# Kernel optimization log

Measured on AMD Instinct MI355X. Metric: run time of the kernel, lower is better.

The kernel has to match this reference:

```python
import jax, jax.numpy as jnp
import numpy as np

B, A, D, H, F = 256, 96, 384, 192, 96   # molecules, atoms, feat, hidden, species-MLP out
S = 4                                   # number of species (H, C, N, O)
E = B * A * 32                          # edges (avg degree 32)
CUTOFF = 5.2


def smooth_cutoff(d, cutoff):
    # Smoothstep-style cutoff: 1 at d=0, smoothly -> 0 at d=cutoff (Smoothstep class, reversed edges)
    x = jnp.clip((cutoff - d) / cutoff, 0.0, 1.0)
    return x ** 3 * (x * (6.0 * x - 15.0) + 10.0)


def setup_inputs() -> dict:
    key = jax.random.key(0)
    ks = jax.random.split(key, 9)
    species = jax.random.randint(ks[0], (B, A), 0, S, dtype=jnp.int32)
    in_features = jax.random.normal(ks[1], (B, A, D), dtype=jnp.float32)
    atom_index12 = jax.random.randint(ks[2], (2, E), 0, B * A, dtype=jnp.int32)
    distances = jax.random.uniform(ks[3], (E,), jnp.float32, 0.1, CUTOFF)
    total_charges = jnp.zeros((B,), jnp.float32)
    W1 = jax.random.normal(ks[4], (S, D, H), jnp.float32) / np.float32(np.sqrt(D))
    W2 = jax.random.normal(ks[5], (S, H, F), jnp.float32) / np.float32(np.sqrt(H))
    Wn = jax.random.normal(ks[6], (S, F, F), jnp.float32) / np.float32(np.sqrt(F))
    Wf = jax.random.normal(ks[7], (S, 2 * F, 1), jnp.float32) / np.float32(np.sqrt(2 * F))
    return dict(species=species, in_features=in_features, atom_index12=atom_index12,
                distances=distances, total_charges=total_charges,
                W1=W1, W2=W2, Wn=Wn, Wf=Wf,
                decay_prefactor=jnp.asarray(1.0, jnp.float32),
                decay_factor=jnp.asarray(1.0, jnp.float32))


def reference(species, in_features, atom_index12, distances, total_charges,
              W1, W2, Wn, Wf, decay_prefactor, decay_factor):
    b, a, d = in_features.shape
    n = b * a
    sp = species.reshape(-1)                      # [N]
    x = in_features.reshape(n, d)                 # [N, D]

    # per-species main MLP dispatch: internal[i] = MLP_{sp[i]}(x[i])
    internal = jnp.zeros((n, F), x.dtype)
    for s in range(S):
        mask = (sp == s)[:, None]
        h = jax.nn.gelu(x @ W1[s]) @ W2[s]        # [N, F]
        internal = internal + jnp.where(mask, h, jnp.zeros((), x.dtype))

    # per-species neighbor MLP
    nbr = jnp.zeros((n, F), x.dtype)
    for s in range(S):
        mask = (sp == s)[:, None]
        nbr = nbr + jnp.where(mask, internal @ Wn[s], jnp.zeros((), x.dtype))

    # distance-decayed edge messages: merged[i0] += nbr[i1]*w, merged[i1] += nbr[i0]*w
    decay = (decay_prefactor ** 2) * jnp.exp(-(decay_factor ** 2) * distances) \
            * smooth_cutoff(distances, CUTOFF)    # [E]
    i0, i1 = atom_index12[0], atom_index12[1]
    m_to_i0 = nbr[i1] * decay[:, None]            # [E, F]
    m_to_i1 = nbr[i0] * decay[:, None]
    merged = jax.ops.segment_sum(jnp.concatenate([m_to_i0, m_to_i1], axis=0),
                                 jnp.concatenate([i0, i1], axis=0),
                                 num_segments=n)  # [N, F]

    feats = jnp.concatenate([internal, merged], axis=-1)  # [N, 2F]

    # per-species final head -> precharges
    precharges = jnp.zeros((n,), x.dtype)
    for s in range(S):
        mask = (sp == s)
        precharges = precharges + jnp.where(mask, (feats @ Wf[s])[:, 0], jnp.zeros((), x.dtype))
    precharges = precharges.reshape(b, a)

    # total-charge redistribution (uniform factors, no learned redistribution)
    dummy_mask = species != -1
    factors = 1.0 / dummy_mask.sum(-1, keepdims=True).astype(x.dtype)
    charges = precharges + (total_charges - precharges.sum(-1))[:, None] * factors
    charges = jnp.where(dummy_mask, charges, jnp.zeros((), x.dtype))
    return species, charges, precharges
```

## Files before the change

kernel.cpp:

```cpp
#include <hip/hip_runtime.h>
#include <cstdint>
#include <cstddef>

#define NBm 256
#define NAm 96
#define NDm 384
#define NHm 192
#define NFm 96
#define NSm 4
#define NATOMS (NBm*NAm)
#define NEe (NATOMS*32)
#define NMSG (2*NEe)
#define HBLK2 768
#define CUTOFF_ 5.2f

typedef __attribute__((ext_vector_type(8))) short short8;
typedef __attribute__((ext_vector_type(4))) float float4v;
typedef __attribute__((ext_vector_type(2))) int int2v;

__device__ __forceinline__ short f2bf(float f){
  union { float f; unsigned u; } v; v.f = f;
  unsigned r = v.u + 0x7FFFu + ((v.u >> 16) & 1u);
  return (short)(r >> 16);
}

__device__ __forceinline__ float gelu_t(float x){
  float u = 0.7978845608028654f * (x + 0.044715f * x*x*x);
  float e = __expf(-2.0f * fabsf(u));
  float t = (1.0f - e) / (1.0f + e);
  t = (u >= 0.f) ? t : -t;
  return 0.5f * x * (1.0f + t);
}

#define W1N (NSm*NDm*NHm)
#define W2N (NSm*NHm*NFm)
#define WNN (NSm*NFm*NFm)
__global__ void k_wprep(const float* __restrict__ W1, const float* __restrict__ W2,
                        const float* __restrict__ Wn,
                        short* __restrict__ W1t, short* __restrict__ W2t,
                        short* __restrict__ Wnt, int* __restrict__ spc){
  if (blockIdx.x == 0 && threadIdx.x < NSm) spc[threadIdx.x] = 0;
  int idx = blockIdx.x*256 + threadIdx.x;
  if (idx < W1N){
    int s = idx / (NDm*NHm); int rem = idx - s*NDm*NHm;
    int k = rem / NHm, c = rem - k*NHm;
    W1t[(s*NHm + c)*NDm + k] = f2bf(W1[idx]);
  } else if (idx < W1N + W2N){
    int j = idx - W1N;
    int s = j / (NHm*NFm); int rem = j - s*NHm*NFm;
    int k = rem / NFm, c = rem - k*NFm;
    W2t[(s*NFm + c)*NHm + k] = f2bf(W2[j]);
  } else if (idx < W1N + W2N + WNN){
    int j = idx - W1N - W2N;
    int s = j / (NFm*NFm); int rem = j - s*NFm*NFm;
    int k = rem / NFm, c = rem - k*NFm;
    Wnt[(s*NFm + c)*NFm + k] = f2bf(Wn[j]);
  }
}

__global__ void k_spcount(const int* __restrict__ sp, int* __restrict__ spc){
  __shared__ int h[NSm];
  int t = threadIdx.x;
  if (t < NSm) h[t] = 0;
  __syncthreads();
  int i = blockIdx.x*256 + t;
  atomicAdd(&h[sp[i]], 1);
  __syncthreads();
  if (t < NSm) atomicAdd(&spc[t], h[t]);
}

__global__ void k_spscan(const int* __restrict__ spc, int* __restrict__ sps, int* __restrict__ spcur){
  if (threadIdx.x==0 && blockIdx.x==0){
    int r=0;
    for (int s=0;s<NSm;s++){ sps[s]=r; spcur[s]=r; r+=spc[s]; }
    sps[NSm]=r;
  }
}

__global__ void k_spscatter(const int* __restrict__ sp, int* __restrict__ spcur,
                            int* __restrict__ order){
  __shared__ int h[NSm], base[NSm];
  int t = threadIdx.x;
  if (t < NSm) h[t]=0;
  __syncthreads();
  int i = blockIdx.x*256 + t;
  int s = sp[i];
  int lr = atomicAdd(&h[s], 1);
  __syncthreads();
  if (t < NSm) base[t] = atomicAdd(&spcur[t], h[t]);
  __syncthreads();
  order[base[s] + lr] = i;
}

__global__ __launch_bounds__(256) void k_mlp(
    const float* __restrict__ X, const int* __restrict__ order,
    const int* __restrict__ sps,
    const short* __restrict__ W1t, const short* __restrict__ W2t,
    const short* __restrict__ Wnt, const float* __restrict__ Wf,
    float* __restrict__ pre, float* __restrict__ nbr_g){
  const int s = blockIdx.y;
  const int s0 = sps[s];
  const int cnt = sps[s+1] - s0;
  const int row0 = blockIdx.x * 64;
  if (row0 >= cnt) return;

  __shared__ short Hs[64][200];
  __shared__ short Is[64][104];
  __shared__ short Ws[19968];
  __shared__ int aids[64];

  const int tid = threadIdx.x;
  if (tid < 64){
    int r = row0 + tid;
    aids[tid] = order[s0 + ((r < cnt) ? r : 0)];
  }
  __syncthreads();

  const int wave = tid >> 6, lane = tid & 63;
  const int lrow = lane & 15, quad = lane >> 4;
  const int arow = wave*16 + lrow;
  const float* xrow = X + (size_t)aids[arow]*NDm + quad*8;

  short8 afs[12];
  #pragma unroll
  for (int kb=0; kb<12; kb++){
    const float* p = xrow + kb*32;
    #pragma unroll
    for (int j=0;j<8;j++) afs[kb][j] = f2bf(p[j]);
  }

  const short* W1s = W1t + (size_t)s*NHm*NDm;
  float4v acc[12];
  #pragma unroll
  for (int i=0;i<12;i++){ acc[i][0]=0.f; acc[i][1]=0.f; acc[i][2]=0.f; acc[i][3]=0.f; }
  for (int kc=0; kc<4; kc++){
    __syncthreads();
    for (int e = tid; e < 192*12; e += 256){
      int c = e / 12, u = e - c*12;
      *(short8*)(&Ws[c*104 + u*8]) = *(const short8*)(W1s + c*NDm + kc*96 + u*8);
    }
    __syncthreads();
    #pragma unroll
    for (int kb3=0; kb3<3; kb3++){
      short8 af = afs[kc*3 + kb3];
      #pragma unroll
      for (int ct=0; ct<12; ct++){
        short8 bfb = *(const short8*)(&Ws[(ct*16 + lrow)*104 + kb3*32 + quad*8]);
        acc[ct] = __builtin_amdgcn_mfma_f32_16x16x32_bf16(af, bfb, acc[ct], 0,0,0);
      }
    }
  }
  #pragma unroll
  for (int ct=0; ct<12; ct++){
    #pragma unroll
    for (int r=0;r<4;r++){
      Hs[wave*16 + quad*4 + r][ct*16 + lrow] = f2bf(gelu_t(acc[ct][r]));
    }
  }

  const short* W2s = W2t + (size_t)s*NFm*NHm;
  float4v acc2[6];
  #pragma unroll
  for (int i=0;i<6;i++){ acc2[i][0]=0.f; acc2[i][1]=0.f; acc2[i][2]=0.f; acc2[i][3]=0.f; }
  __syncthreads();
  for (int e = tid; e < 96*24; e += 256){
    int c = e / 24, u = e - c*24;
    *(short8*)(&Ws[c*200 + u*8]) = *(const short8*)(W2s + c*NHm + u*8);
  }
  __syncthreads();
  for (int kb=0; kb<6; kb++){
    short8 af2 = *(const short8*)(&Hs[wave*16 + lrow][kb*32 + quad*8]);
    #pragma unroll
    for (int ct=0; ct<6; ct++){
      short8 bfb = *(const short8*)(&Ws[(ct*16 + lrow)*200 + kb*32 + quad*8]);
      acc2[ct] = __builtin_amdgcn_mfma_f32_16x16x32_bf16(af2, bfb, acc2[ct], 0,0,0);
    }
  }
  #pragma unroll
  for (int ct=0; ct<6; ct++){
    #pragma unroll
    for (int r=0;r<4;r++){
      Is[wave*16 + quad*4 + r][ct*16 + lrow] = f2bf(acc2[ct][r]);
    }
  }

  {
    float pr[4] = {0.f,0.f,0.f,0.f};
    #pragma unroll
    for (int ct=0; ct<6; ct++){
      float wv = Wf[s*2*NFm + ct*16 + lrow];
      #pragma unroll
      for (int r=0;r<4;r++) pr[r] += acc2[ct][r] * wv;
    }
    #pragma unroll
    for (int m=1; m<16; m<<=1){
      #pragma unroll
      for (int r=0;r<4;r++) pr[r] += __shfl_xor(pr[r], m, 64);
    }
    if (lrow == 0){
      #pragma unroll
      for (int r=0;r<4;r++){
        int row = wave*16 + quad*4 + r;
        if (row0 + row < cnt) pre[aids[row]] = pr[r];
      }
    }
  }

  const short* Wns = Wnt + (size_t)s*NFm*NFm;
  float4v acc3[6];
  #pragma unroll
  for (int i=0;i<6;i++){ acc3[i][0]=0.f; acc3[i][1]=0.f; acc3[i][2]=0.f; acc3[i][3]=0.f; }
  __syncthreads();
  for (int e = tid; e < 96*12; e += 256){
    int c = e / 12, u = e - c*12;
    *(short8*)(&Ws[c*104 + u*8]) = *(const short8*)(Wns + c*NFm + u*8);
  }
  __syncthreads();
  for (int kb=0; kb<3; kb++){
    short8 af3 = *(const short8*)(&Is[wave*16 + lrow][kb*32 + quad*8]);
    #pragma unroll
    for (int ct=0; ct<6; ct++){
      short8 bfb = *(const short8*)(&Ws[(ct*16 + lrow)*104 + kb*32 + quad*8]);
      acc3[ct] = __builtin_amdgcn_mfma_f32_16x16x32_bf16(af3, bfb, acc3[ct], 0,0,0);
    }
  }
  #pragma unroll
  for (int ct=0; ct<6; ct++){
    #pragma unroll
    for (int r=0;r<4;r++){
      int row = wave*16 + quad*4 + r, col = ct*16 + lrow;
      if (row0 + row < cnt) nbr_g[(size_t)aids[row]*NFm + col] = acc3[ct][r];
    }
  }
}

__global__ void k_nd4(const float* __restrict__ nbr, const float* __restrict__ Wf,
                      float* __restrict__ nd4){
  int a = blockIdx.x*4 + (threadIdx.x >> 6);
  int lane = threadIdx.x & 63;
  bool lo = lane < 32;
  const float* np = nbr + (size_t)a*NFm;
  float nv1 = np[lane];
  float nv2 = lo ? np[64+lane] : 0.f;
  const float* w0 = Wf + 0*2*NFm + NFm;
  const float* w1 = Wf + 1*2*NFm + NFm;
  const float* w2 = Wf + 2*2*NFm + NFm;
  const float* w3 = Wf + 3*2*NFm + NFm;
  float n0 = nv1*w0[lane] + (lo ? nv2*w0[64+lane] : 0.f);
  float n1 = nv1*w1[lane] + (lo ? nv2*w1[64+lane] : 0.f);
  float n2 = nv1*w2[lane] + (lo ? nv2*w2[64+lane] : 0.f);
  float n3 = nv1*w3[lane] + (lo ? nv2*w3[64+lane] : 0.f);
  #pragma unroll
  for (int m=1; m<64; m<<=1){
    n0 += __shfl_xor(n0, m, 64);
    n1 += __shfl_xor(n1, m, 64);
    n2 += __shfl_xor(n2, m, 64);
    n3 += __shfl_xor(n3, m, 64);
  }
  if (lane == 0){
    float4v v; v[0]=n0; v[1]=n1; v[2]=n2; v[3]=n3;
    *(float4v*)(nd4 + (size_t)a*4) = v;
  }
}

__global__ __launch_bounds__(1024) void k_hist(const int* __restrict__ ai,
                                               int* __restrict__ Hist){
  __shared__ int h[NBm];
  int t = threadIdx.x;
  if (t < NBm) h[t] = 0;
  __syncthreads();
  int base = blockIdx.x*2048;
  atomicAdd(&h[ai[base + t] / NAm], 1);
  atomicAdd(&h[ai[base + 1024 + t] / NAm], 1);
  __syncthreads();
  if (t < NBm) Hist[blockIdx.x*NBm + t] = h[t];
}

__global__ void k_mscan(int* __restrict__ Hist, int* __restrict__ Tot){
  __shared__ int sums[256];
  int mol = blockIdx.x, t = threadIdx.x;
  int v[3]; int loc = 0;
  #pragma unroll
  for (int j=0;j<3;j++){ v[j] = Hist[(t*3+j)*NBm + mol]; loc += v[j]; }
  sums[t] = loc; __syncthreads();
  for (int off=1; off<256; off<<=1){
    int x = (t >= off) ? sums[t-off] : 0;
    __syncthreads();
    sums[t] += x;
    __syncthreads();
  }
  int run = sums[t] - loc;
  #pragma unroll
  for (int j=0;j<3;j++){ Hist[(t*3+j)*NBm + mol] = run; run += v[j]; }
  if (t == 255) Tot[mol] = run;
}

__global__ void k_segscan(const int* __restrict__ Tot, int* __restrict__ Seg){
  __shared__ int s[256];
  int t = threadIdx.x;
  int v = Tot[t]; s[t] = v; __syncthreads();
  for (int off=1; off<256; off<<=1){
    int x = (t >= off) ? s[t-off] : 0;
    __syncthreads();
    s[t] += x;
    __syncthreads();
  }
  Seg[t] = s[t] - v;
  if (t == 255) Seg[256] = s[255];
}

__global__ __launch_bounds__(1024) void k_scatter(const int* __restrict__ ai,
    const float* __restrict__ dist, const float* __restrict__ pref,
    const float* __restrict__ fac, const int* __restrict__ Hist,
    const int* __restrict__ Seg, int2v* __restrict__ Msg){
  __shared__ int cnt[NBm];
  __shared__ int off[NBm];
  int t = threadIdx.x;
  if (t < NBm){ cnt[t] = 0; off[t] = Seg[t] + Hist[blockIdx.x*NBm + t]; }
  __syncthreads();
  int base = blockIdx.x*2048;
  float p = pref[0], fc = fac[0];
  #pragma unroll
  for (int half=0; half<2; half++){
    int m = base + half*1024 + t;
    int dest = ai[m];
    int other = ai[(m < NEe) ? m + NEe : m - NEe];
    int e = (m < NEe) ? m : m - NEe;
    float d = dist[e];
    float x = (CUTOFF_ - d) * (1.0f/CUTOFF_);
    x = fminf(fmaxf(x, 0.f), 1.f);
    float sc = x*x*x*(x*(6.f*x - 15.f) + 10.f);
    float w = p*p * expf(-fc*fc*d) * sc;
    int mol = dest / NAm, dl = dest - mol*NAm;
    int rank = atomicAdd(&cnt[mol], 1);
    int2v msg; msg[0] = (other << 7) | dl; msg[1] = __float_as_int(w);
    Msg[off[mol] + rank] = msg;
  }
}

__global__ __launch_bounds__(1024) void k_accum(const int* __restrict__ Seg,
    const int2v* __restrict__ Msg, const float* __restrict__ nd4,
    const int* __restrict__ sp, const float* __restrict__ pre,
    const float* __restrict__ tc, float* __restrict__ out){
  __shared__ float acc[NAm];
  __shared__ int spl[NAm];
  __shared__ float red[128];
  int mol = blockIdx.x, t = threadIdx.x;
  if (t < NAm){ acc[t] = 0.f; spl[t] = sp[mol*NAm + t]; }
  __syncthreads();
  int s0 = Seg[mol], s1 = Seg[mol+1];
  for (int i = s0 + t; i < s1; i += 1024){
    int2v kw = Msg[i];
    int key = kw[0]; float w = __int_as_float(kw[1]);
    int dl = key & 127, other = key >> 7;
    float val = w * nd4[(size_t)other*4 + spl[dl]];
    atomicAdd(&acc[dl], val);
  }
  __syncthreads();
  float pch = 0.f;
  if (t < NAm) pch = pre[mol*NAm + t] + acc[t];
  if (t < 128) red[t] = (t < NAm) ? pch : 0.f;
  __syncthreads();
  for (int o=64; o>0; o>>=1){
    if (t < o) red[t] += red[t + o];
    __syncthreads();
  }
  float sum = red[0];
  if (t < NAm){
    float c = pch + (tc[mol] - sum) * (1.0f/96.0f);
    out[mol*NAm + t] = (float)spl[t];
    out[NATOMS + mol*NAm + t] = c;
    out[2*NATOMS + mol*NAm + t] = pch;
  }
}

extern "C" void kernel_launch(void* const* d_in, const int* in_sizes, int n_in,
                              void* d_out, int out_size, void* d_ws, size_t ws_size,
                              hipStream_t stream) {
  const int*   species = (const int*)  d_in[0];
  const float* X       = (const float*)d_in[1];
  const int*   ai      = (const int*)  d_in[2];
  const float* dist    = (const float*)d_in[3];
  const float* tc      = (const float*)d_in[4];
  const float* W1      = (const float*)d_in[5];
  const float* W2      = (const float*)d_in[6];
  const float* Wn      = (const float*)d_in[7];
  const float* Wf      = (const float*)d_in[8];
  const float* pref    = (const float*)d_in[9];
  const float* fac     = (const float*)d_in[10];
  float* out = (float*)d_out;

  char* w = (char*)d_ws;
  auto alloc = [&](size_t bytes)->char*{
    char* p = w; w += (bytes + 255) & ~(size_t)255; return p;
  };
  int*   spc   = (int*)  alloc(64);
  int*   sps   = (int*)  alloc(64);
  int*   spcur = (int*)  alloc(64);
  int*   order = (int*)  alloc((size_t)NATOMS*4);
  float* nd4   = (float*)alloc((size_t)NATOMS*4*4);
  float* pre   = (float*)alloc((size_t)NATOMS*4);
  float* nbr   = (float*)alloc((size_t)NATOMS*NFm*4);
  short* W1t   = (short*)alloc((size_t)W1N*2);
  short* W2t   = (short*)alloc((size_t)W2N*2);
  short* Wnt   = (short*)alloc((size_t)WNN*2);
  int*   Hist  = (int*)  alloc((size_t)HBLK2*NBm*4);
  int*   Tot   = (int*)  alloc(1024);
  int*   Seg   = (int*)  alloc((NBm+1)*4);
  int2v* Msg   = (int2v*)alloc((size_t)NMSG*8);

  k_wprep<<<(W1N+W2N+WNN)/256, 256, 0, stream>>>(W1, W2, Wn, W1t, W2t, Wnt, spc);
  k_spcount<<<NATOMS/256, 256, 0, stream>>>(species, spc);
  k_spscan<<<1, 64, 0, stream>>>(spc, sps, spcur);
  k_spscatter<<<NATOMS/256, 256, 0, stream>>>(species, spcur, order);
  dim3 g(NATOMS/64, NSm);
  k_mlp<<<g, 256, 0, stream>>>(X, order, sps, W1t, W2t, Wnt, Wf, pre, nbr);
  k_nd4<<<NATOMS/4, 256, 0, stream>>>(nbr, Wf, nd4);
  k_hist<<<HBLK2, 1024, 0, stream>>>(ai, Hist);
  k_mscan<<<NBm, 256, 0, stream>>>(Hist, Tot);
  k_segscan<<<1, 256, 0, stream>>>(Tot, Seg);
  k_scatter<<<HBLK2, 1024, 0, stream>>>(ai, dist, pref, fac, Hist, Seg, Msg);
  k_accum<<<NBm, 1024, 0, stream>>>(Seg, Msg, nd4, species, pre, tc, out);
}
```

Measured before the change: 182.6 us.

## Replace sort-by-molecule edge pipeline with direct global atomic accumulation

Drops the histogram, scan and scatter kernels that bucketed messages by molecule. Each edge now computes its decay weight once and atomically adds both directed contributions straight into a global per-atom buffer, which is zeroed inside the weight-prep kernel. This removes several launches and the 12.6 MB message buffer write and read. In exchange it relies on global float atomics on random addresses, which can contend and makes the summation order nondeterministic.

New measurement: 253.1 us. 1.39x slower.

```diff
diff --git a/kernel.cpp b/kernel.cpp
--- a/kernel.cpp
+++ b/kernel.cpp
@@ -10,13 +10,10 @@
 #define NSm 4
 #define NATOMS (NBm*NAm)
 #define NEe (NATOMS*32)
-#define NMSG (2*NEe)
-#define HBLK2 768
 #define CUTOFF_ 5.2f
 
 typedef __attribute__((ext_vector_type(8))) short short8;
 typedef __attribute__((ext_vector_type(4))) float float4v;
-typedef __attribute__((ext_vector_type(2))) int int2v;
 
 __device__ __forceinline__ short f2bf(float f){
   union { float f; unsigned u; } v; v.f = f;
@@ -35,10 +32,12 @@
 #define W1N (NSm*NDm*NHm)
 #define W2N (NSm*NHm*NFm)
 #define WNN (NSm*NFm*NFm)
+#define WTOT (W1N+W2N+WNN)
 __global__ void k_wprep(const float* __restrict__ W1, const float* __restrict__ W2,
                         const float* __restrict__ Wn,
                         short* __restrict__ W1t, short* __restrict__ W2t,
-                        short* __restrict__ Wnt, int* __restrict__ spc){
+                        short* __restrict__ Wnt, int* __restrict__ spc,
+                        float* __restrict__ mrg){
   if (blockIdx.x == 0 && threadIdx.x < NSm) spc[threadIdx.x] = 0;
   int idx = blockIdx.x*256 + threadIdx.x;
   if (idx < W1N){
@@ -50,11 +49,14 @@
     int s = j / (NHm*NFm); int rem = j - s*NHm*NFm;
     int k = rem / NFm, c = rem - k*NFm;
     W2t[(s*NFm + c)*NHm + k] = f2bf(W2[j]);
-  } else if (idx < W1N + W2N + WNN){
+  } else if (idx < WTOT){
     int j = idx - W1N - W2N;
     int s = j / (NFm*NFm); int rem = j - s*NFm*NFm;
     int k = rem / NFm, c = rem - k*NFm;
     Wnt[(s*NFm + c)*NFm + k] = f2bf(Wn[j]);
+  } else {
+    int z = idx - WTOT;
+    mrg[z] = 0.f;
   }
 }
 
@@ -263,103 +265,37 @@
   }
 }
 
-__global__ __launch_bounds__(1024) void k_hist(const int* __restrict__ ai,
-                                               int* __restrict__ Hist){
-  __shared__ int h[NBm];
-  int t = threadIdx.x;
-  if (t < NBm) h[t] = 0;
-  __syncthreads();
-  int base = blockIdx.x*2048;
-  atomicAdd(&h[ai[base + t] / NAm], 1);
-  atomicAdd(&h[ai[base + 1024 + t] / NAm], 1);
-  __syncthreads();
-  if (t < NBm) Hist[blockIdx.x*NBm + t] = h[t];
-}
-
-__global__ void k_mscan(int* __restrict__ Hist, int* __restrict__ Tot){
-  __shared__ int sums[256];
-  int mol = blockIdx.x, t = threadIdx.x;
-  int v[3]; int loc = 0;
-  #pragma unroll
-  for (int j=0;j<3;j++){ v[j] = Hist[(t*3+j)*NBm + mol]; loc += v[j]; }
-  sums[t] = loc; __syncthreads();
-  for (int off=1; off<256; off<<=1){
-    int x = (t >= off) ? sums[t-off] : 0;
-    __syncthreads();
-    sums[t] += x;
-    __syncthreads();
-  }
-  int run = sums[t] - loc;
-  #pragma unroll
-  for (int j=0;j<3;j++){ Hist[(t*3+j)*NBm + mol] = run; run += v[j]; }
-  if (t == 255) Tot[mol] = run;
-}
-
-__global__ void k_segscan(const int* __restrict__ Tot, int* __restrict__ Seg){
-  __shared__ int s[256];
-  int t = threadIdx.x;
-  int v = Tot[t]; s[t] = v; __syncthreads();
-  for (int off=1; off<256; off<<=1){
-    int x = (t >= off) ? s[t-off] : 0;
-    __syncthreads();
-    s[t] += x;
-    __syncthreads();
-  }
-  Seg[t] = s[t] - v;
-  if (t == 255) Seg[256] = s[255];
-}
-
-__global__ __launch_bounds__(1024) void k_scatter(const int* __restrict__ ai,
+__global__ __launch_bounds__(256) void k_edges(const int* __restrict__ ai,
     const float* __restrict__ dist, const float* __restrict__ pref,
-    const float* __restrict__ fac, const int* __restrict__ Hist,
-    const int* __restrict__ Seg, int2v* __restrict__ Msg){
-  __shared__ int cnt[NBm];
-  __shared__ int off[NBm];
-  int t = threadIdx.x;
-  if (t < NBm){ cnt[t] = 0; off[t] = Seg[t] + Hist[blockIdx.x*NBm + t]; }
-  __syncthreads();
-  int base = blockIdx.x*2048;
+    const float* __restrict__ fac, const int* __restrict__ sp,
+    const float* __restrict__ nd4, float* __restrict__ mrg){
+  int e = blockIdx.x*256 + threadIdx.x;
+  int i0 = ai[e];
+  int i1 = ai[NEe + e];
+  float d = dist[e];
   float p = pref[0], fc = fac[0];
-  #pragma unroll
-  for (int half=0; half<2; half++){
-    int m = base + half*1024 + t;
-    int dest = ai[m];
-    int other = ai[(m < NEe) ? m + NEe : m - NEe];
-    int e = (m < NEe) ? m : m - NEe;
-    float d = dist[e];
-    float x = (CUTOFF_ - d) * (1.0f/CUTOFF_);
-    x = fminf(fmaxf(x, 0.f), 1.f);
-    float sc = x*x*x*(x*(6.f*x - 15.f) + 10.f);
-    float w = p*p * expf(-fc*fc*d) * sc;
-    int mol = dest / NAm, dl = dest - mol*NAm;
-    int rank = atomicAdd(&cnt[mol], 1);
-    int2v msg; msg[0] = (other << 7) | dl; msg[1] = __float_as_int(w);
-    Msg[off[mol] + rank] = msg;
-  }
-}
-
-__global__ __launch_bounds__(1024) void k_accum(const int* __restrict__ Seg,
-    const int2v* __restrict__ Msg, const float* __restrict__ nd4,
-    const int* __restrict__ sp, const float* __restrict__ pre,
+  float x = (CUTOFF_ - d) * (1.0f/CUTOFF_);
+  x = fminf(fmaxf(x, 0.f), 1.f);
+  float sc = x*x*x*(x*(6.f*x - 15.f) + 10.f);
+  float w = p*p * expf(-fc*fc*d) * sc;
+  int s0 = sp[i0], s1 = sp[i1];
+  float v0 = w * nd4[(size_t)i1*4 + s0];
+  float v1 = w * nd4[(size_t)i0*4 + s1];
+  atomicAdd(&mrg[i0], v0);
+  atomicAdd(&mrg[i1], v1);
+}
+
+__global__ __launch_bounds__(128) void k_final(const float* __restrict__ pre,
+    const float* __restrict__ mrg, const int* __restrict__ sp,
     const float* __restrict__ tc, float* __restrict__ out){
-  __shared__ float acc[NAm];
-  __shared__ int spl[NAm];
   __shared__ float red[128];
   int mol = blockIdx.x, t = threadIdx.x;
-  if (t < NAm){ acc[t] = 0.f; spl[t] = sp[mol*NAm + t]; }
-  __syncthreads();
-  int s0 = Seg[mol], s1 = Seg[mol+1];
-  for (int i = s0 + t; i < s1; i += 1024){
-    int2v kw = Msg[i];
-    int key = kw[0]; float w = __int_as_float(kw[1]);
-    int dl = key & 127, other = key >> 7;
-    float val = w * nd4[(size_t)other*4 + spl[dl]];
-    atomicAdd(&acc[dl], val);
-  }
-  __syncthreads();
-  float pch = 0.f;
-  if (t < NAm) pch = pre[mol*NAm + t] + acc[t];
-  if (t < 128) red[t] = (t < NAm) ? pch : 0.f;
+  float pch = 0.f; int s = 0;
+  if (t < NAm){
+    s = sp[mol*NAm + t];
+    pch = pre[mol*NAm + t] + mrg[mol*NAm + t];
+  }
+  red[t] = (t < NAm) ? pch : 0.f;
   __syncthreads();
   for (int o=64; o>0; o>>=1){
     if (t < o) red[t] += red[t + o];
@@ -367,9 +303,8 @@
   }
   float sum = red[0];
   if (t < NAm){
-    float c = pch + (tc[mol] - sum) * (1.0f/96.0f);
-    out[mol*NAm + t] = (float)spl[t];
-    out[NATOMS + mol*NAm + t] = c;
+    out[mol*NAm + t] = (float)s;
+    out[NATOMS + mol*NAm + t] = pch + (tc[mol] - sum) * (1.0f/96.0f);
     out[2*NATOMS + mol*NAm + t] = pch;
   }
 }
@@ -400,25 +335,19 @@
   int*   order = (int*)  alloc((size_t)NATOMS*4);
   float* nd4   = (float*)alloc((size_t)NATOMS*4*4);
   float* pre   = (float*)alloc((size_t)NATOMS*4);
+  float* mrg   = (float*)alloc((size_t)NATOMS*4);
   float* nbr   = (float*)alloc((size_t)NATOMS*NFm*4);
   short* W1t   = (short*)alloc((size_t)W1N*2);
   short* W2t   = (short*)alloc((size_t)W2N*2);
   short* Wnt   = (short*)alloc((size_t)WNN*2);
-  int*   Hist  = (int*)  alloc((size_t)HBLK2*NBm*4);
-  int*   Tot   = (int*)  alloc(1024);
-  int*   Seg   = (int*)  alloc((NBm+1)*4);
-  int2v* Msg   = (int2v*)alloc((size_t)NMSG*8);
-
-  k_wprep<<<(W1N+W2N+WNN)/256, 256, 0, stream>>>(W1, W2, Wn, W1t, W2t, Wnt, spc);
+
+  k_wprep<<<WTOT/256 + NATOMS/256, 256, 0, stream>>>(W1, W2, Wn, W1t, W2t, Wnt, spc, mrg);
   k_spcount<<<NATOMS/256, 256, 0, stream>>>(species, spc);
   k_spscan<<<1, 64, 0, stream>>>(spc, sps, spcur);
   k_spscatter<<<NATOMS/256, 256, 0, stream>>>(species, spcur, order);
   dim3 g(NATOMS/64, NSm);
   k_mlp<<<g, 256, 0, stream>>>(X, order, sps, W1t, W2t, Wnt, Wf, pre, nbr);
   k_nd4<<<NATOMS/4, 256, 0, stream>>>(nbr, Wf, nd4);
-  k_hist<<<HBLK2, 1024, 0, stream>>>(ai, Hist);
-  k_mscan<<<NBm, 256, 0, stream>>>(Hist, Tot);
-  k_segscan<<<1, 256, 0, stream>>>(Tot, Seg);
-  k_scatter<<<HBLK2, 1024, 0, stream>>>(ai, dist, pref, fac, Hist, Seg, Msg);
-  k_accum<<<NBm, 1024, 0, stream>>>(Seg, Msg, nd4, species, pre, tc, out);
-}
+  k_edges<<<NEe/256, 256, 0, stream>>>(ai, dist, pref, fac, species, nd4, mrg);
+  k_final<<<NBm, 128, 0, stream>>>(pre, mrg, species, tc, out);
+}
```
